# Kernel optimization log

Measured on AMD Instinct MI355X. Metric: run time of the kernel, lower is better.

## Reference

```python
import jax, jax.numpy as jnp
import numpy as np

TOP_K = 2

def setup_inputs() -> dict:
    key = jax.random.key(0)
    k1, k2, k3 = jax.random.split(key, 3)
    B, S, H, E = 4, 4096, 4096, 64
    return {
        "hidden_states": jax.random.normal(k1, (B, S, H), dtype=jnp.float32),
        "weight": jax.random.normal(k2, (E, H), dtype=jnp.float32),
        "bias": jax.random.normal(k3, (E,), dtype=jnp.float32),
    }

def reference(hidden_states, weight, bias):
    B, S, H = hidden_states.shape
    E = weight.shape[0]
    x = hidden_states.reshape(-1, H)                      # [N, H]
    router_logits = jnp.einsum('nh,eh->ne', x, weight) + bias  # [N, E]
    routing_weights, selected_experts = jax.lax.top_k(router_logits, TOP_K)
    routing_weights = jax.nn.softmax(routing_weights.astype(jnp.float32), axis=-1).astype(hidden_states.dtype)
    N = x.shape[0]
    rows = jnp.arange(N)[:, None]
    final = jnp.zeros((N, E), dtype=router_logits.dtype).at[rows, selected_experts].set(routing_weights)
    return final.reshape(B, S, E), selected_experts
```

## Files before the change

### kernel.cpp

```cpp
#include <hip/hip_runtime.h>
#include <math.h>


constexpr int E_EXPERTS = 64;
constexpr int H_DIM = 4096;
constexpr int BLOCK = 512;
constexpr int ROWS_B = 64;
constexpr int NSTEP = 64;
constexpr int KHALF = 2048;
constexpr int SROW = 40;
constexpr int PSTR = E_EXPERTS * SROW;
constexpr int QSTR = 3 * PSTR;
constexpr int BSTR = 2 * QSTR;
constexpr int W_ELEMS = E_EXPERTS * H_DIM;

typedef __attribute__((ext_vector_type(8))) short short8;
typedef __attribute__((ext_vector_type(4))) float f32x4;

__device__ __forceinline__ float4 ld4(const float* p) {
  return *reinterpret_cast<const float4*>(p);
}
__device__ __forceinline__ short8 lds8(const unsigned short* p) {
  return *reinterpret_cast<const short8*>(p);
}

__device__ __forceinline__ void block_barrier() {
  asm volatile("s_waitcnt lgkmcnt(0)" ::: "memory");
  __builtin_amdgcn_s_barrier();
}

__device__ __forceinline__ unsigned short bf_rne(float x) {
  unsigned u = __builtin_bit_cast(unsigned, x);
  return (unsigned short)((u + 0x7fffu + ((u >> 16) & 1u)) >> 16);
}
__device__ __forceinline__ float bf2f(unsigned short b) {
  return __builtin_bit_cast(float, ((unsigned)b) << 16);
}
__device__ __forceinline__ void split3(float x, unsigned short& h,
                                       unsigned short& m, unsigned short& l) {
  unsigned short hb = (unsigned short)(__builtin_bit_cast(unsigned, x) >> 16);
  float r1 = x - bf2f(hb);
  unsigned short mb = (unsigned short)(__builtin_bit_cast(unsigned, r1) >> 16);
  float r2 = r1 - bf2f(mb);
  h = hb;
  m = mb;
  l = bf_rne(r2);
}
__device__ __forceinline__ void split3_8(float4 a, float4 b, short8& h,
                                         short8& m, short8& l) {
  unsigned short hh, mm, ll;
  split3(a.x, hh, mm, ll); h[0] = (short)hh; m[0] = (short)mm; l[0] = (short)ll;
  split3(a.y, hh, mm, ll); h[1] = (short)hh; m[1] = (short)mm; l[1] = (short)ll;
  split3(a.z, hh, mm, ll); h[2] = (short)hh; m[2] = (short)mm; l[2] = (short)ll;
  split3(a.w, hh, mm, ll); h[3] = (short)hh; m[3] = (short)mm; l[3] = (short)ll;
  split3(b.x, hh, mm, ll); h[4] = (short)hh; m[4] = (short)mm; l[4] = (short)ll;
  split3(b.y, hh, mm, ll); h[5] = (short)hh; m[5] = (short)mm; l[5] = (short)ll;
  split3(b.z, hh, mm, ll); h[6] = (short)hh; m[6] = (short)mm; l[6] = (short)ll;
  split3(b.w, hh, mm, ll); h[7] = (short)hh; m[7] = (short)mm; l[7] = (short)ll;
}

__global__ __launch_bounds__(256) void split_w_kernel(
    const float* __restrict__ w, unsigned short* __restrict__ wh,
    unsigned short* __restrict__ wm, unsigned short* __restrict__ wl) {
  const int i = (blockIdx.x * 256 + threadIdx.x) * 4;
  float4 v = ld4(w + i);
  ushort4 h4, m4, l4;
  split3(v.x, h4.x, m4.x, l4.x);
  split3(v.y, h4.y, m4.y, l4.y);
  split3(v.z, h4.z, m4.z, l4.z);
  split3(v.w, h4.w, m4.w, l4.w);
  *reinterpret_cast<ushort4*>(wh + i) = h4;
  *reinterpret_cast<ushort4*>(wm + i) = m4;
  *reinterpret_cast<ushort4*>(wl + i) = l4;
}

__global__ __launch_bounds__(BLOCK, 2) void topk_router_mfma(
    const float* __restrict__ x, const unsigned short* __restrict__ wh,
    const unsigned short* __restrict__ wm,
    const unsigned short* __restrict__ wl, const float* __restrict__ bias,
    float* __restrict__ out_final, float* __restrict__ out_idx) {
  __shared__ short smem[2 * BSTR];

  const int tid = threadIdx.x;
  const int lane = tid & 63;
  const int wid = tid >> 6;
  const int rg = wid & 3;
  const int kq = wid >> 2;
  const int rowBase = blockIdx.x * ROWS_B;
  const int lr = lane & 15;
  const int kg = lane >> 4;

  const int sw = tid & 255;
  const int se = sw >> 2;
  const int sk8 = tid & 3;
  const int skq = tid >> 8;
  const size_t gbase = (size_t)se * H_DIM + skq * KHALF + sk8 * 8;
  const int lbase = skq * QSTR + se * SROW + sk8 * 8;

  const float* __restrict__ xp =
      x + (size_t)(rowBase + rg * 16 + lr) * H_DIM + kq * KHALF + kg * 8;

  short8 s0, s1, s2;
  float4 xA0, xA1, xB0, xB1;

  f32x4 acc0 = {0.f, 0.f, 0.f, 0.f}, acc1 = acc0, acc2 = acc0, acc3 = acc0;

#define SLOAD(s)                        \
  do {                                  \
    const size_t go = gbase + (s) * 32; \
    s0 = lds8(wh + go);                 \
    s1 = lds8(wm + go);                 \
    s2 = lds8(wl + go);                 \
  } while (0)

#define SWRITE(buf)                                                         \
  do {                                                                      \
    *reinterpret_cast<short8*>(&smem[(buf)*BSTR + lbase + 0 * PSTR]) = s0;  \
    *reinterpret_cast<short8*>(&smem[(buf)*BSTR + lbase + 1 * PSTR]) = s1;  \
    *reinterpret_cast<short8*>(&smem[(buf)*BSTR + lbase + 2 * PSTR]) = s2;  \
  } while (0)

#define XLOAD(d0, d1, s)                  \
  do {                                    \
    d0 = ld4(xp + (size_t)(s) * 32);      \
    d1 = ld4(xp + (size_t)(s) * 32 + 4);  \
  } while (0)

  SLOAD(0);
  SWRITE(0);
  SLOAD(1);
  XLOAD(xA0, xA1, 0);
  XLOAD(xB0, xB1, 1);
  block_barrier();

  const int fbase = kq * QSTR + lr * SROW + kg * 8;

#define FRAGS(buf, g, p)                      \
  (*reinterpret_cast<const short8*>(          \
      &smem[(buf)*BSTR + fbase + (g)*16 * SROW + (p)*PSTR]))

#define MM(d, a, b) d = __builtin_amdgcn_mfma_f32_16x16x32_bf16(a, b, d, 0, 0, 0)
#define PROD6(d, Ah, Am, Al, Bh, Bm, Bl)                      \
  MM(d, Ah, Bh); MM(d, Ah, Bm); MM(d, Am, Bh); MM(d, Am, Bm); \
  MM(d, Ah, Bl); MM(d, Al, Bh)

#define PHASE(s, buf, XF0, XF1)                                     \
  do {                                                              \
    if ((s) + 1 < NSTEP) SWRITE(1 - (buf));  \
    if ((s) + 2 < NSTEP) SLOAD((s) + 2);       \
    short8 b0h = FRAGS(buf, 0, 0), b0m = FRAGS(buf, 0, 1),          \
           b0l = FRAGS(buf, 0, 2);                                  \
    short8 b1h = FRAGS(buf, 1, 0), b1m = FRAGS(buf, 1, 1),          \
           b1l = FRAGS(buf, 1, 2);                                  \
    short8 b2h = FRAGS(buf, 2, 0), b2m = FRAGS(buf, 2, 1),          \
           b2l = FRAGS(buf, 2, 2);                                  \
    short8 b3h = FRAGS(buf, 3, 0), b3m = FRAGS(buf, 3, 1),          \
           b3l = FRAGS(buf, 3, 2);                                  \
    short8 ah, am, al;                                              \
    split3_8(XF0, XF1, ah, am, al);                                 \
    if ((s) + 2 < NSTEP) XLOAD(XF0, XF1, (s) + 2);                  \
    PROD6(acc0, ah, am, al, b0h, b0m, b0l);                         \
    PROD6(acc1, ah, am, al, b1h, b1m, b1l);                         \
    PROD6(acc2, ah, am, al, b2h, b2m, b2l);                         \
    PROD6(acc3, ah, am, al, b3h, b3m, b3l);                         \
    block_barrier();                                                \
  } while (0)

  for (int s = 0; s < NSTEP; s += 2) {
    PHASE(s, 0, xA0, xA1);
    PHASE(s + 1, 1, xB0, xB1);
  }

  float* part = reinterpret_cast<float*>(smem);
  const int pr = kg * 4;
#define PSTORE(A, g)                                                       \
  part[((size_t)kq * 64 + rg * 16 + pr + 0) * 68 + (g)*16 + lr] = A[0];    \
  part[((size_t)kq * 64 + rg * 16 + pr + 1) * 68 + (g)*16 + lr] = A[1];    \
  part[((size_t)kq * 64 + rg * 16 + pr + 2) * 68 + (g)*16 + lr] = A[2];    \
  part[((size_t)kq * 64 + rg * 16 + pr + 3) * 68 + (g)*16 + lr] = A[3];
  PSTORE(acc0, 0)
  PSTORE(acc1, 1)
  PSTORE(acc2, 2)
  PSTORE(acc3, 3)
  block_barrier();

  const int r = tid >> 3;
  const int eb = (tid & 7) * 8;
  const int n = rowBase + r;

  float v8[8];
#pragma unroll
  for (int j = 0; j < 8; ++j) {
    int e = eb + j;
    v8[j] = (part[(size_t)r * 68 + e] + part[(size_t)(64 + r) * 68 + e]) +
            bias[e];
  }

  float av = -INFINITY, bv = -INFINITY;
  int ai = E_EXPERTS, bi = E_EXPERTS;
#pragma unroll
  for (int j = 0; j < 8; ++j) {
    int e = eb + j;
    float v = v8[j];
    bool beats_a = (v > av) || (v == av && e < ai);
    bool beats_b = (v > bv) || (v == bv && e < bi);
    if (beats_a) {
      bv = av; bi = ai; av = v; ai = e;
    } else if (beats_b) {
      bv = v; bi = e;
    }
  }
#pragma unroll
  for (int d = 1; d < 8; d <<= 1) {
    float av2 = __shfl_xor(av, d);
    float bv2 = __shfl_xor(bv, d);
    int ai2 = __shfl_xor(ai, d);
    int bi2 = __shfl_xor(bi, d);
    bool afirst = (av > av2) || (av == av2 && ai < ai2);
    float na, nb;
    int nai, nbi;
    if (afirst) {
      na = av; nai = ai;
      bool t = (bv > av2) || (bv == av2 && bi < ai2);
      nb = t ? bv : av2;
      nbi = t ? bi : ai2;
    } else {
      na = av2; nai = ai2;
      bool t = (av > bv2) || (av == bv2 && ai < bi2);
      nb = t ? av : bv2;
      nbi = t ? ai : bi2;
    }
    av = na; ai = nai; bv = nb; bi = nbi;
  }

  float e1 = expf(bv - av);
  float denom = 1.0f + e1;
  float p0 = 1.0f / denom;
  float p1 = e1 / denom;

#pragma unroll
  for (int i = 0; i < 2; ++i) {
    float4 o4;
    float* po = &o4.x;
#pragma unroll
    for (int j = 0; j < 4; ++j) {
      int e = eb + i * 4 + j;
      po[j] = (e == ai) ? p0 : (e == bi) ? p1 : 0.0f;
    }
    *reinterpret_cast<float4*>(&out_final[(size_t)n * E_EXPERTS + eb + i * 4]) =
        o4;
  }
  if ((tid & 7) == 0) {
    out_idx[(size_t)n * 2 + 0] = (float)ai;
    out_idx[(size_t)n * 2 + 1] = (float)bi;
  }
}

extern "C" void kernel_launch(void* const* d_in, const int* in_sizes, int n_in,
                              void* d_out, int out_size, void* d_ws,
                              size_t ws_size, hipStream_t stream) {
  const float* x = (const float*)d_in[0];
  const float* w = (const float*)d_in[1];
  const float* bias = (const float*)d_in[2];
  const int N = in_sizes[0] / H_DIM;
  float* out_final = (float*)d_out;
  float* out_idx = out_final + (size_t)N * E_EXPERTS;

  unsigned short* wh = (unsigned short*)d_ws;
  unsigned short* wm = wh + W_ELEMS;
  unsigned short* wl = wm + W_ELEMS;

  split_w_kernel<<<W_ELEMS / (256 * 4), 256, 0, stream>>>(w, wh, wm, wl);
  topk_router_mfma<<<N / ROWS_B, BLOCK, 0, stream>>>(x, wh, wm, wl, bias,
                                                     out_final, out_idx);
}
```

Before: 101.2 us.

## Remap waves to 4-way K split with 32 rows each for B-fragment reuse

Changes the wave decomposition from 4 row groups x 2 K halves to 2 row halves x 4 K quarters, so each wave computes 32 rows and reuses each LDS weight fragment across two A tiles. Each phase now stages a wider weight slice (four K quarters, six loads per thread), and the loop runs half as many phases, so there are fewer barriers. The cost is more accumulator and x registers per thread, a larger LDS footprint (about 120KB, which may conflict with 2 blocks per CU), and a four-way partial-sum reduction at the end.

```diff
diff --git a/kernel.cpp b/kernel.cpp
--- a/kernel.cpp
+++ b/kernel.cpp
@@ -6,12 +6,10 @@
 constexpr int H_DIM = 4096;
 constexpr int BLOCK = 512;
 constexpr int ROWS_B = 64;
-constexpr int NSTEP = 64;
-constexpr int KHALF = 2048;
+constexpr int NPH = 32;
+constexpr int KSLICE = 1024;
 constexpr int SROW = 40;
-constexpr int PSTR = E_EXPERTS * SROW;
-constexpr int QSTR = 3 * PSTR;
-constexpr int BSTR = 2 * QSTR;
+constexpr int BUFS = 12 * 64 * SROW;
 constexpr int W_ELEMS = E_EXPERTS * H_DIM;
 
 typedef __attribute__((ext_vector_type(8))) short short8;
@@ -79,109 +77,140 @@
     const unsigned short* __restrict__ wm,
     const unsigned short* __restrict__ wl, const float* __restrict__ bias,
     float* __restrict__ out_final, float* __restrict__ out_idx) {
-  __shared__ short smem[2 * BSTR];
+  __shared__ short smem[2 * BUFS];
 
   const int tid = threadIdx.x;
   const int lane = tid & 63;
   const int wid = tid >> 6;
-  const int rg = wid & 3;
-  const int kq = wid >> 2;
+  const int kq = wid & 3;
+  const int rh = wid >> 2;
   const int rowBase = blockIdx.x * ROWS_B;
   const int lr = lane & 15;
   const int kg = lane >> 4;
 
-  const int sw = tid & 255;
-  const int se = sw >> 2;
-  const int sk8 = tid & 3;
-  const int skq = tid >> 8;
-  const size_t gbase = (size_t)se * H_DIM + skq * KHALF + sk8 * 8;
-  const int lbase = skq * QSTR + se * SROW + sk8 * 8;
-
-  const float* __restrict__ xp =
-      x + (size_t)(rowBase + rg * 16 + lr) * H_DIM + kq * KHALF + kg * 8;
-
-  short8 s0, s1, s2;
-  float4 xA0, xA1, xB0, xB1;
-
-  f32x4 acc0 = {0.f, 0.f, 0.f, 0.f}, acc1 = acc0, acc2 = acc0, acc3 = acc0;
-
-#define SLOAD(s)                        \
-  do {                                  \
-    const size_t go = gbase + (s) * 32; \
-    s0 = lds8(wh + go);                 \
-    s1 = lds8(wm + go);                 \
-    s2 = lds8(wl + go);                 \
-  } while (0)
-
-#define SWRITE(buf)                                                         \
-  do {                                                                      \
-    *reinterpret_cast<short8*>(&smem[(buf)*BSTR + lbase + 0 * PSTR]) = s0;  \
-    *reinterpret_cast<short8*>(&smem[(buf)*BSTR + lbase + 1 * PSTR]) = s1;  \
-    *reinterpret_cast<short8*>(&smem[(buf)*BSTR + lbase + 2 * PSTR]) = s2;  \
-  } while (0)
-
-#define XLOAD(d0, d1, s)                  \
-  do {                                    \
-    d0 = ld4(xp + (size_t)(s) * 32);      \
-    d1 = ld4(xp + (size_t)(s) * 32 + 4);  \
-  } while (0)
+#define DECL_UNIT(i)                                                       \
+  const int u##i = tid + 512 * (i);                                        \
+  const int pq##i = u##i >> 8;                                             \
+  const int kqs##i = pq##i / 3;                                            \
+  const int pl##i = pq##i - kqs##i * 3;                                    \
+  const unsigned short* gp##i =                                            \
+      (pl##i == 0 ? wh : (pl##i == 1 ? wm : wl)) +                         \
+      (size_t)((u##i >> 2) & 63) * H_DIM + kqs##i * KSLICE + (u##i & 3) * 8; \
+  const int lo##i = (pq##i * 64 + ((u##i >> 2) & 63)) * SROW + (u##i & 3) * 8; \
+  short8 sv##i;
+  DECL_UNIT(0) DECL_UNIT(1) DECL_UNIT(2)
+  DECL_UNIT(3) DECL_UNIT(4) DECL_UNIT(5)
+
+#define SLOAD(t)                                  \
+  do {                                            \
+    sv0 = lds8(gp0 + (size_t)(t) * 32);           \
+    sv1 = lds8(gp1 + (size_t)(t) * 32);           \
+    sv2 = lds8(gp2 + (size_t)(t) * 32);           \
+    sv3 = lds8(gp3 + (size_t)(t) * 32);           \
+    sv4 = lds8(gp4 + (size_t)(t) * 32);           \
+    sv5 = lds8(gp5 + (size_t)(t) * 32);           \
+  } while (0)
+
+#define SWRITE(buf)                                                    \
+  do {                                                                 \
+    *reinterpret_cast<short8*>(&smem[(buf)*BUFS + lo0]) = sv0;         \
+    *reinterpret_cast<short8*>(&smem[(buf)*BUFS + lo1]) = sv1;         \
+    *reinterpret_cast<short8*>(&smem[(buf)*BUFS + lo2]) = sv2;         \
+    *reinterpret_cast<short8*>(&smem[(buf)*BUFS + lo3]) = sv3;         \
+    *reinterpret_cast<short8*>(&smem[(buf)*BUFS + lo4]) = sv4;         \
+    *reinterpret_cast<short8*>(&smem[(buf)*BUFS + lo5]) = sv5;         \
+  } while (0)
+
+  const float* __restrict__ xr0 =
+      x + (size_t)(rowBase + rh * 32 + lr) * H_DIM + kq * KSLICE + kg * 8;
+  const float* __restrict__ xr1 = xr0 + (size_t)16 * H_DIM;
+
+  float4 xA0, xA1, xA2, xA3, xB0, xB1, xB2, xB3;
+#define XLOADA(t)                                \
+  do {                                           \
+    xA0 = ld4(xr0 + (size_t)(t) * 32);           \
+    xA1 = ld4(xr0 + (size_t)(t) * 32 + 4);       \
+    xA2 = ld4(xr1 + (size_t)(t) * 32);           \
+    xA3 = ld4(xr1 + (size_t)(t) * 32 + 4);       \
+  } while (0)
+#define XLOADB(t)                                \
+  do {                                           \
+    xB0 = ld4(xr0 + (size_t)(t) * 32);           \
+    xB1 = ld4(xr0 + (size_t)(t) * 32 + 4);       \
+    xB2 = ld4(xr1 + (size_t)(t) * 32);           \
+    xB3 = ld4(xr1 + (size_t)(t) * 32 + 4);       \
+  } while (0)
+
+  f32x4 accA0 = {0.f, 0.f, 0.f, 0.f}, accA1 = accA0, accA2 = accA0,
+        accA3 = accA0, accB0 = accA0, accB1 = accA0, accB2 = accA0,
+        accB3 = accA0;
 
   SLOAD(0);
   SWRITE(0);
   SLOAD(1);
-  XLOAD(xA0, xA1, 0);
-  XLOAD(xB0, xB1, 1);
+  XLOADA(0);
+  XLOADB(1);
   block_barrier();
 
-  const int fbase = kq * QSTR + lr * SROW + kg * 8;
-
-#define FRAGS(buf, g, p)                      \
-  (*reinterpret_cast<const short8*>(          \
-      &smem[(buf)*BSTR + fbase + (g)*16 * SROW + (p)*PSTR]))
+#define FRAG(buf, eg, pl)                                              \
+  (*reinterpret_cast<const short8*>(                                   \
+      &smem[(buf)*BUFS + ((kq * 3 + (pl)) * 64 + (eg)*16 + lr) * SROW + \
+            kg * 8]))
 
 #define MM(d, a, b) d = __builtin_amdgcn_mfma_f32_16x16x32_bf16(a, b, d, 0, 0, 0)
 #define PROD6(d, Ah, Am, Al, Bh, Bm, Bl)                      \
   MM(d, Ah, Bh); MM(d, Ah, Bm); MM(d, Am, Bh); MM(d, Am, Bm); \
   MM(d, Ah, Bl); MM(d, Al, Bh)
 
-#define PHASE(s, buf, XF0, XF1)                                     \
-  do {                                                              \
-    if ((s) + 1 < NSTEP) SWRITE(1 - (buf));  \
-    if ((s) + 2 < NSTEP) SLOAD((s) + 2);       \
-    short8 b0h = FRAGS(buf, 0, 0), b0m = FRAGS(buf, 0, 1),          \
-           b0l = FRAGS(buf, 0, 2);                                  \
-    short8 b1h = FRAGS(buf, 1, 0), b1m = FRAGS(buf, 1, 1),          \
-           b1l = FRAGS(buf, 1, 2);                                  \
-    short8 b2h = FRAGS(buf, 2, 0), b2m = FRAGS(buf, 2, 1),          \
-           b2l = FRAGS(buf, 2, 2);                                  \
-    short8 b3h = FRAGS(buf, 3, 0), b3m = FRAGS(buf, 3, 1),          \
-           b3l = FRAGS(buf, 3, 2);                                  \
-    short8 ah, am, al;                                              \
-    split3_8(XF0, XF1, ah, am, al);                                 \
-    if ((s) + 2 < NSTEP) XLOAD(XF0, XF1, (s) + 2);                  \
-    PROD6(acc0, ah, am, al, b0h, b0m, b0l);                         \
-    PROD6(acc1, ah, am, al, b1h, b1m, b1l);                         \
-    PROD6(acc2, ah, am, al, b2h, b2m, b2l);                         \
-    PROD6(acc3, ah, am, al, b3h, b3m, b3l);                         \
-    block_barrier();                                                \
-  } while (0)
-
-  for (int s = 0; s < NSTEP; s += 2) {
-    PHASE(s, 0, xA0, xA1);
-    PHASE(s + 1, 1, xB0, xB1);
+#define PHASE(p, buf, X0, X1, X2, X3, XLOADM)                        \
+  do {                                                               \
+    if ((p) + 1 < NPH) SWRITE((buf) ^ 1);    \
+    if ((p) + 2 < NPH) SLOAD((p) + 2);        \
+    short8 b0h = FRAG(buf, 0, 0), b0m = FRAG(buf, 0, 1),             \
+           b0l = FRAG(buf, 0, 2);                                    \
+    short8 b1h = FRAG(buf, 1, 0), b1m = FRAG(buf, 1, 1),             \
+           b1l = FRAG(buf, 1, 2);                                    \
+    short8 b2h = FRAG(buf, 2, 0), b2m = FRAG(buf, 2, 1),             \
+           b2l = FRAG(buf, 2, 2);                                    \
+    short8 b3h = FRAG(buf, 3, 0), b3m = FRAG(buf, 3, 1),             \
+           b3l = FRAG(buf, 3, 2);                                    \
+    short8 ah0, am0, al0, ah1, am1, al1;                             \
+    split3_8(X0, X1, ah0, am0, al0);                                 \
+    split3_8(X2, X3, ah1, am1, al1);                                 \
+    if ((p) + 2 < NPH) XLOADM((p) + 2);     \
+    PROD6(accA0, ah0, am0, al0, b0h, b0m, b0l);                      \
+    PROD6(accA1, ah0, am0, al0, b1h, b1m, b1l);                      \
+    PROD6(accA2, ah0, am0, al0, b2h, b2m, b2l);                      \
+    PROD6(accA3, ah0, am0, al0, b3h, b3m, b3l);                      \
+    PROD6(accB0, ah1, am1, al1, b0h, b0m, b0l);                      \
+    PROD6(accB1, ah1, am1, al1, b1h, b1m, b1l);                      \
+    PROD6(accB2, ah1, am1, al1, b2h, b2m, b2l);                      \
+    PROD6(accB3, ah1, am1, al1, b3h, b3m, b3l);                      \
+    block_barrier();                                                 \
+  } while (0)
+
+  for (int p = 0; p < NPH; p += 2) {
+    PHASE(p, 0, xA0, xA1, xA2, xA3, XLOADA);
+    PHASE(p + 1, 1, xB0, xB1, xB2, xB3, XLOADB);
   }
 
   float* part = reinterpret_cast<float*>(smem);
   const int pr = kg * 4;
-#define PSTORE(A, g)                                                       \
-  part[((size_t)kq * 64 + rg * 16 + pr + 0) * 68 + (g)*16 + lr] = A[0];    \
-  part[((size_t)kq * 64 + rg * 16 + pr + 1) * 68 + (g)*16 + lr] = A[1];    \
-  part[((size_t)kq * 64 + rg * 16 + pr + 2) * 68 + (g)*16 + lr] = A[2];    \
-  part[((size_t)kq * 64 + rg * 16 + pr + 3) * 68 + (g)*16 + lr] = A[3];
-  PSTORE(acc0, 0)
-  PSTORE(acc1, 1)
-  PSTORE(acc2, 2)
-  PSTORE(acc3, 3)
+  const int rwA = rh * 32 + pr;
+  const int rwB = rh * 32 + 16 + pr;
+#define PSTORE(A, rw, g)                                              \
+  part[(size_t)(kq * 64 + (rw) + 0) * 68 + (g)*16 + lr] = A[0];       \
+  part[(size_t)(kq * 64 + (rw) + 1) * 68 + (g)*16 + lr] = A[1];       \
+  part[(size_t)(kq * 64 + (rw) + 2) * 68 + (g)*16 + lr] = A[2];       \
+  part[(size_t)(kq * 64 + (rw) + 3) * 68 + (g)*16 + lr] = A[3];
+  PSTORE(accA0, rwA, 0)
+  PSTORE(accA1, rwA, 1)
+  PSTORE(accA2, rwA, 2)
+  PSTORE(accA3, rwA, 3)
+  PSTORE(accB0, rwB, 0)
+  PSTORE(accB1, rwB, 1)
+  PSTORE(accB2, rwB, 2)
+  PSTORE(accB3, rwB, 3)
   block_barrier();
 
   const int r = tid >> 3;
@@ -192,7 +221,10 @@
 #pragma unroll
   for (int j = 0; j < 8; ++j) {
     int e = eb + j;
-    v8[j] = (part[(size_t)r * 68 + e] + part[(size_t)(64 + r) * 68 + e]) +
+    v8[j] = ((part[(size_t)(0 * 64 + r) * 68 + e] +
+              part[(size_t)(1 * 64 + r) * 68 + e]) +
+             (part[(size_t)(2 * 64 + r) * 68 + e] +
+              part[(size_t)(3 * 64 + r) * 68 + e])) +
             bias[e];
   }
 
```

Result: faster. 91.70 us (-9.4%).
